# Kernel tuning notes

Measured on AMD Instinct MI355X. Metric: run time of the kernel, lower is better.

Reference implementation:

```python
import jax, jax.numpy as jnp
import numpy as np

O, T, DIN, H, DOUT = 50000, 500000, 128, 256, 128


def setup_inputs() -> dict:
    key = jax.random.key(0)
    ks = jax.random.split(key, 12)
    s = 0.05
    return {
        "obj_vecs": jax.random.normal(ks[0], (O, DIN), jnp.float32),
        "pred_vecs": jax.random.normal(ks[1], (T, DIN), jnp.float32),
        "edges": jax.random.randint(ks[2], (T, 2), 0, O, jnp.int64),
        "w1a": jax.random.normal(ks[3], (3 * DIN, H), jnp.float32) * s,
        "b1a": jax.random.normal(ks[4], (H,), jnp.float32) * s,
        "w1b": jax.random.normal(ks[5], (H, 2 * H + DOUT), jnp.float32) * s,
        "b1b": jax.random.normal(ks[6], (2 * H + DOUT,), jnp.float32) * s,
        "w2a": jax.random.normal(ks[7], (H, H), jnp.float32) * s,
        "b2a": jax.random.normal(ks[8], (H,), jnp.float32) * s,
        "w2b": jax.random.normal(ks[9], (H, DOUT), jnp.float32) * s,
        "b2b": jax.random.normal(ks[10], (DOUT,), jnp.float32) * s,
    }


def reference(obj_vecs, pred_vecs, edges, w1a, b1a, w1b, b1b, w2a, b2a, w2b, b2b):
    n_obj = obj_vecs.shape[0]
    h_dim = w2a.shape[0]
    d_out = w2b.shape[1]
    s_idx = edges[:, 0]
    o_idx = edges[:, 1]
    # gather subject/object node features, concat with predicate: [T, 3*Din]
    cur_t = jnp.concatenate([obj_vecs[s_idx], pred_vecs, obj_vecs[o_idx]], axis=1)
    # edge MLP (net1): Linear-ReLU-Linear-ReLU -> [T, 2H + Dout]
    new_t = jax.nn.relu(jax.nn.relu(cur_t @ w1a + b1a) @ w1b + b1b)
    new_s = new_t[:, :h_dim]
    new_p = new_t[:, h_dim:h_dim + d_out]
    new_o = new_t[:, h_dim + d_out:]
    # scatter-add pooling back to nodes, both endpoints
    idx = jnp.concatenate([s_idx, o_idx])
    vals = jnp.concatenate([new_s, new_o], axis=0)
    pooled = jax.ops.segment_sum(vals, idx, num_segments=n_obj)
    # avg pooling: divide by per-node incidence count (clamped to >= 1)
    counts = jax.ops.segment_sum(jnp.ones(idx.shape[0], obj_vecs.dtype), idx,
                                 num_segments=n_obj)
    pooled = pooled / jnp.clip(counts, 1.0)[:, None]
    # node MLP (net2)
    new_obj = jax.nn.relu(jax.nn.relu(pooled @ w2a + b2a) @ w2b + b2b)
    return new_obj, new_p
```

## Files before the change

### kernel.cpp

```cpp
#include <hip/hip_runtime.h>


using f32x4 = __attribute__((ext_vector_type(4))) float;
using s16x8 = __attribute__((ext_vector_type(8))) short;
typedef unsigned short u16x8 __attribute__((ext_vector_type(8)));

#define VMCNT4  asm volatile("s_waitcnt vmcnt(4)" ::: "memory")
#define VMCNT8  asm volatile("s_waitcnt vmcnt(8)" ::: "memory")
#define VMCNT16 asm volatile("s_waitcnt vmcnt(16)" ::: "memory")
#define VMCNT20 asm volatile("s_waitcnt vmcnt(20)" ::: "memory")
#define VMCNT36 asm volatile("s_waitcnt vmcnt(36)" ::: "memory")
#define LGKM0   asm volatile("s_waitcnt lgkmcnt(0)" ::: "memory")
#define BAR     __builtin_amdgcn_s_barrier()
#define SCHEDB  __builtin_amdgcn_sched_barrier(0)

static __device__ __forceinline__ unsigned short f2b(float f) {
    unsigned int u = __float_as_uint(f);
    unsigned int r = (u + 0x7fffu + ((u >> 16) & 1u)) >> 16;
    return (unsigned short)r;
}

static __device__ __forceinline__ unsigned f2bpk(float lo, float hi) {
    unsigned r;
    asm("v_cvt_pk_bf16_f32 %0, %1, %2" : "=v"(r) : "v"(lo), "v"(hi));
    return r;
}

static __device__ __forceinline__ float b2f(unsigned short b) {
    return __uint_as_float(((unsigned)b) << 16);
}

static __device__ __forceinline__ unsigned swz(unsigned row, unsigned byteoff) {
    return byteoff ^ ((row & 7u) << 4);
}

static __device__ __forceinline__ void gload_lds16(const unsigned short* g, unsigned short* l) {
    __builtin_amdgcn_global_load_lds(
        (const __attribute__((address_space(1))) unsigned int*)g,
        (__attribute__((address_space(3))) unsigned int*)l,
        16, 0, 0);
}

#define PREP_ELEMS (98304 + 163840 + 65536 + 32768)

__global__ void prep_count_kernel(const float* __restrict__ w1a, const float* __restrict__ w1b,
                                  const float* __restrict__ w2a, const float* __restrict__ w2b,
                                  unsigned short* __restrict__ w1aT, unsigned short* __restrict__ w1bT,
                                  unsigned short* __restrict__ w2aT, unsigned short* __restrict__ w2bT,
                                  const int* __restrict__ edges, int* __restrict__ cnt,
                                  int* __restrict__ slotS, int* __restrict__ slotO, int T) {
    int t = blockIdx.x * blockDim.x + threadIdx.x;
    if (t >= PREP_ELEMS) {
        int e = t - PREP_ELEMS;
        if (e < T) {
            slotS[e] = atomicAdd(&cnt[edges[2 * (long long)e]], 1);
            slotO[e] = atomicAdd(&cnt[edges[2 * (long long)e + 1]], 1);
        }
        return;
    }
    if (t < 6 * 16384) {
        int kt = t >> 14;
        int rem = t & 16383; int c = rem >> 6, kk = rem & 63;
        unsigned byte = ((unsigned)(c * 128 + kk * 2)) ^ ((c & 7u) << 4);
        *(unsigned short*)((char*)w1aT + (size_t)kt * 32768 + byte) =
            f2b(w1a[(size_t)(kt * 64 + kk) * 256 + c]);
        return;
    }
    t -= 98304;
    if (t < 10 * 16384) {
        int tile = t >> 14; int nc = tile >> 1, kh = tile & 1;
        int rem = t & 16383; int c = rem >> 7, kk = rem & 127;
        unsigned byte = ((unsigned)(c * 256 + kk * 2)) ^ ((c & 7u) << 4);
        *(unsigned short*)((char*)w1bT + (size_t)tile * 32768 + byte) =
            f2b(w1b[(size_t)(kh * 128 + kk) * 640 + nc * 128 + c]);
        return;
    }
    t -= 163840;
    if (t < 65536) { int n = t >> 8, k = t & 255; w2aT[t] = f2b(w2a[k * 256 + n]); return; }
    t -= 65536;
    if (t < 32768) { int n = t >> 8, k = t & 255; w2bT[t] = f2b(w2b[k * 128 + n]); return; }
}

__global__ void scan_kernel(const int* __restrict__ cnt, int* __restrict__ rowptr, int O) {
    __shared__ int sc[1024];
    const int tid = threadIdx.x;
    const int per = (O + 1023) >> 10;
    const int base = tid * per;
    int s = 0;
    for (int i = 0; i < per; ++i) { int j = base + i; if (j < O) s += cnt[j]; }
    sc[tid] = s;
    __syncthreads();
    for (int d = 1; d < 1024; d <<= 1) {
        int v = (tid >= d) ? sc[tid - d] : 0;
        __syncthreads();
        sc[tid] += v;
        __syncthreads();
    }
    int off = sc[tid] - s;
    for (int i = 0; i < per; ++i) {
        int j = base + i;
        if (j < O) { rowptr[j] = off; off += cnt[j]; }
    }
    if (tid == 0) rowptr[O] = sc[1023];
}

__global__ __launch_bounds__(512, 2) void edge_mlp(
    const float* __restrict__ obj, const float* __restrict__ pred,
    const int* __restrict__ edges,
    const unsigned short* __restrict__ w1aT, const float* __restrict__ b1a,
    const unsigned short* __restrict__ w1bT, const float* __restrict__ b1b,
    const int* __restrict__ slotS, const int* __restrict__ slotO,
    const int* __restrict__ rowptr,
    unsigned short* __restrict__ edgeout, float* __restrict__ outP, int T) {
    const int m0 = blockIdx.x * 128;
    const int tid = threadIdx.x;
    const int lane = tid & 63, wid = tid >> 6;
    const int wm = wid >> 2, wn = wid & 3;
    const bool evenL = ((lane & 1) == 0);

    __shared__ unsigned short U[81920];
    char* const ldsb = (char*)U;
    char* const bbase = ldsb + 65536;

    bool okR[4][4];
    #pragma unroll
    for (int mi = 0; mi < 4; ++mi)
        #pragma unroll
        for (int rr = 0; rr < 4; ++rr)
            okR[mi][rr] = (m0 + wm * 64 + mi * 16 + ((lane >> 4) << 2) + rr) < T;

    int slotSr[4][2], slotOr[4][2];
    #pragma unroll
    for (int mi = 0; mi < 4; ++mi)
        #pragma unroll
        for (int k = 0; k < 2; ++k) {
            int rsel = evenL ? k : 2 + k;
            int e = m0 + wm * 64 + mi * 16 + ((lane >> 4) << 2) + rsel;
            if (e >= T) e = T - 1;
            int si = edges[2 * (long long)e];
            int oi = edges[2 * (long long)e + 1];
            slotSr[mi][k] = slotS[e] + rowptr[si];
            slotOr[mi][k] = slotO[e] + rowptr[oi];
        }

    const int r = tid >> 2;
    const int q = tid & 3;
    int e_r = m0 + r; if (e_r >= T) e_r = T - 1;
    const int sIdx_r = edges[2 * (long long)e_r];
    const int oIdx_r = edges[2 * (long long)e_r + 1];

    float bias1[4], bias2[5][2];
    #pragma unroll
    for (int nj = 0; nj < 4; ++nj) bias1[nj] = b1a[wn * 64 + nj * 16 + (lane & 15)];
    #pragma unroll
    for (int nc = 0; nc < 5; ++nc)
        #pragma unroll
        for (int nj = 0; nj < 2; ++nj)
            bias2[nc][nj] = b1b[nc * 128 + wn * 32 + nj * 16 + (lane & 15)];

    #pragma unroll
    for (int mi = 0; mi < 4; ++mi)
        #pragma unroll
        for (int k = 0; k < 2; ++k)
            asm volatile("" :: "v"(slotSr[mi][k]), "v"(slotOr[mi][k]));
    #pragma unroll
    for (int nj = 0; nj < 4; ++nj) asm volatile("" :: "v"(bias1[nj]));
    #pragma unroll
    for (int nc = 0; nc < 5; ++nc)
        #pragma unroll
        for (int nj = 0; nj < 2; ++nj) asm volatile("" :: "v"(bias2[nc][nj]));
    asm volatile("" :: "v"((float)sIdx_r), "v"((float)oIdx_r));
    SCHEDB;

    auto aSrc = [&](int kt) -> const float4* {
        const float* s;
        if (kt < 2)      s = obj  + (long long)sIdx_r * 128 + kt * 64;
        else if (kt < 4) s = pred + (long long)e_r   * 128 + (kt - 2) * 64;
        else             s = obj  + (long long)oIdx_r * 128 + (kt - 4) * 64;
        return (const float4*)s;
    };

    auto tp = [&](int i) -> const unsigned short* {
        return (i < 6) ? (w1aT + (size_t)i * 16384) : (w1bT + (size_t)(i - 6) * 16384);
    };

    auto stage32 = [&](const unsigned short* gt, char* bb) {
        #pragma unroll
        for (int rr4 = 0; rr4 < 4; ++rr4) {
            unsigned off = wid * 4096u + rr4 * 1024u;
            gload_lds16((const unsigned short*)((const char*)gt + off + lane * 16u),
                        (unsigned short*)(bb + off));
        }
    };

    auto writeA = [&](const float4* ap, char* ab) {
        #pragma unroll
        for (int i = 0; i < 4; ++i) {
            float4 v = ap[i];
            uint2 pk;
            pk.x = f2bpk(v.x, v.y);
            pk.y = f2bpk(v.z, v.w);
            unsigned byte = (r * 128u + q * 32u + i * 8u) ^ ((r & 7u) << 4);
            *(uint2*)(ab + byte) = pk;
        }
    };

    f32x4 acc1[4][4];
    #pragma unroll
    for (int a = 0; a < 4; ++a)
        #pragma unroll
        for (int b = 0; b < 4; ++b) acc1[a][b] = f32x4{0.f, 0.f, 0.f, 0.f};

    auto mfma1 = [&](const char* ab, const char* bb) {
        #pragma unroll
        for (int ks = 0; ks < 2; ++ks) {
            const unsigned kk = ks * 32u + ((lane >> 4) << 3);
            s16x8 af[4];
            #pragma unroll
            for (int mi = 0; mi < 4; ++mi) {
                unsigned row = wm * 64u + mi * 16u + (lane & 15);
                af[mi] = *(const s16x8*)(ab + ((row * 128u + kk * 2u) ^ ((row & 7u) << 4)));
            }
            #pragma unroll
            for (int nj = 0; nj < 4; ++nj) {
                unsigned c = wn * 64u + nj * 16u + (lane & 15);
                s16x8 bf = *(const s16x8*)(bb + ((c * 128u + kk * 2u) ^ ((c & 7u) << 4)));
                #pragma unroll
                for (int mi = 0; mi < 4; ++mi)
                    acc1[mi][nj] = __builtin_amdgcn_mfma_f32_16x16x32_bf16(af[mi], bf, acc1[mi][nj], 0, 0, 0);
            }
        }
    };

    float4 ap[4];
    {
        const float4* s4 = aSrc(0);
        #pragma unroll
        for (int i = 0; i < 4; ++i) ap[i] = s4[q * 4 + i];
    }
    writeA(ap, ldsb);
    stage32(tp(0), bbase);
    stage32(tp(1), bbase + 32768);
    {
        const float4* s4 = aSrc(1);
        #pragma unroll
        for (int i = 0; i < 4; ++i) ap[i] = s4[q * 4 + i];
    }
    VMCNT8;
    LGKM0; BAR; SCHEDB;

    #pragma unroll
    for (int s = 0; s < 6; ++s) {
        stage32(tp(s + 2), bbase + ((s + 2) % 3) * 32768);
        __builtin_amdgcn_s_setprio(1);
        mfma1(ldsb + ((s >> 0) & 1) * 16384, bbase + (s % 3) * 32768);
        __builtin_amdgcn_s_setprio(0);
        VMCNT4;
        if (s < 5) {
            writeA(ap, ldsb + ((s + 1) & 1) * 16384);
            if (s < 4) {
                const float4* s4 = aSrc(s + 2);
                #pragma unroll
                for (int i = 0; i < 4; ++i) ap[i] = s4[q * 4 + i];
            }
        }
        LGKM0; BAR; SCHEDB;
    }

    #pragma unroll
    for (int nj = 0; nj < 4; ++nj) {
        unsigned col = wn * 64u + nj * 16u + (lane & 15);
        #pragma unroll
        for (int mi = 0; mi < 4; ++mi) {
            float r0 = fmaxf(acc1[mi][nj][0] + bias1[nj], 0.f);
            float r1 = fmaxf(acc1[mi][nj][1] + bias1[nj], 0.f);
            float r2 = fmaxf(acc1[mi][nj][2] + bias1[nj], 0.f);
            float r3 = fmaxf(acc1[mi][nj][3] + bias1[nj], 0.f);
            unsigned p01 = f2bpk(r0, r1);
            unsigned p23 = f2bpk(r2, r3);
            unsigned rowb = wm * 64u + mi * 16u + ((lane >> 4) << 2);
            *(unsigned short*)(ldsb + ((rowb * 512u + col * 2u) ^ ((rowb & 7u) << 4))) = (unsigned short)p01;
            *(unsigned short*)(ldsb + (((rowb + 1) * 512u + col * 2u) ^ (((rowb + 1) & 7u) << 4))) = (unsigned short)(p01 >> 16);
            *(unsigned short*)(ldsb + (((rowb + 2) * 512u + col * 2u) ^ (((rowb + 2) & 7u) << 4))) = (unsigned short)p23;
            *(unsigned short*)(ldsb + (((rowb + 3) * 512u + col * 2u) ^ (((rowb + 3) & 7u) << 4))) = (unsigned short)(p23 >> 16);
        }
    }
    LGKM0; BAR; SCHEDB;

    #pragma unroll
    for (int nc = 0; nc < 5; ++nc) {
        f32x4 acc2[4][2];
        #pragma unroll
        for (int a = 0; a < 4; ++a)
            #pragma unroll
            for (int b = 0; b < 2; ++b) acc2[a][b] = f32x4{0.f, 0.f, 0.f, 0.f};

        #pragma unroll
        for (int kh = 0; kh < 2; ++kh) {
            const int s = 6 + nc * 2 + kh;
            if (s + 2 <= 15) stage32(tp(s + 2), bbase + ((s + 2) % 3) * 32768);
            const char* bb = bbase + (s % 3) * 32768;
            __builtin_amdgcn_s_setprio(1);
            #pragma unroll
            for (int ks = 0; ks < 4; ++ks) {
                const unsigned kkB = ks * 32u + ((lane >> 4) << 3);
                const unsigned kkH = (kh * 128u) + kkB;
                s16x8 af[4];
                #pragma unroll
                for (int mi = 0; mi < 4; ++mi) {
                    unsigned row = wm * 64u + mi * 16u + (lane & 15);
                    af[mi] = *(const s16x8*)(ldsb + ((row * 512u + kkH * 2u) ^ ((row & 7u) << 4)));
                }
                #pragma unroll
                for (int nj = 0; nj < 2; ++nj) {
                    unsigned c = wn * 32u + nj * 16u + (lane & 15);
                    s16x8 bf = *(const s16x8*)(bb + ((c * 256u + kkB * 2u) ^ ((c & 7u) << 4)));
                    #pragma unroll
                    for (int mi = 0; mi < 4; ++mi)
                        acc2[mi][nj] = __builtin_amdgcn_mfma_f32_16x16x32_bf16(af[mi], bf, acc2[mi][nj], 0, 0, 0);
                }
            }
            __builtin_amdgcn_s_setprio(0);

            if (kh == 0) {
                if (s == 6)       { VMCNT4; }
                else if (s == 12) { VMCNT36; }
                else if (s == 14) { VMCNT16; }
                else              { VMCNT20; }
                LGKM0; BAR; SCHEDB;
            }
        }

        if (nc == 2) {
            #pragma unroll
            for (int nj = 0; nj < 2; ++nj) {
                int col = 2 * 128 + wn * 32 + nj * 16 + (lane & 15);
                #pragma unroll
                for (int mi = 0; mi < 4; ++mi)
                    #pragma unroll
                    for (int rr = 0; rr < 4; ++rr) {
                        int row = wm * 64 + mi * 16 + ((lane >> 4) << 2) + rr;
                        if (okR[mi][rr]) {
                            float v = acc2[mi][nj][rr] + bias2[2][nj];
                            v = v > 0.f ? v : 0.f;
                            outP[(long long)(m0 + row) * 128 + (col - 256)] = v;
                        }
                    }
            }
            VMCNT36;
            LGKM0; BAR; SCHEDB;
        } else {
            #pragma unroll
            for (int nj = 0; nj < 2; ++nj) {
                int col = nc * 128 + wn * 32 + nj * 16 + (lane & 15);
                int pc = (nc < 2) ? col : (col - 384);
                int pcb = (lane & 1) ? (pc - 1) : pc;
                #pragma unroll
                for (int mi = 0; mi < 4; ++mi) {
                    float vv[4];
                    #pragma unroll
                    for (int rr = 0; rr < 4; ++rr) {
                        float v = acc2[mi][nj][rr] + bias2[nc][nj];
                        vv[rr] = v > 0.f ? v : 0.f;
                    }
                    float nb0 = __shfl_xor(vv[0], 1);
                    float nb1 = __shfl_xor(vv[1], 1);
                    float nb2 = __shfl_xor(vv[2], 1);
                    float nb3 = __shfl_xor(vv[3], 1);
                    #pragma unroll
                    for (int k = 0; k < 2; ++k) {
                        float lo = evenL ? (k ? vv[1] : vv[0]) : (k ? nb3 : nb2);
                        float hi = evenL ? (k ? nb1 : nb0) : (k ? vv[3] : vv[2]);
                        int rsel = evenL ? k : 2 + k;
                        if (okR[mi][rsel]) {
                            int slot = (nc < 2) ? slotSr[mi][k] : slotOr[mi][k];
                            unsigned pk = f2bpk(lo, hi);
                            *(unsigned*)(edgeout + (size_t)slot * 256 + pcb) = pk;
                        }
                    }
                }
            }
            if (nc < 4) {
                VMCNT20;
                LGKM0; BAR; SCHEDB;
            }
        }
    }
}

__global__ __launch_bounds__(256, 3) void obj_mlp(
    const unsigned short* __restrict__ edgeout, const int* __restrict__ rowptr,
    const unsigned short* __restrict__ w2aT, const float* __restrict__ b2a,
    const unsigned short* __restrict__ w2bT, const float* __restrict__ b2b,
    float* __restrict__ outObj, int O) {
    const int m0 = blockIdx.x * 64;
    const int tid = threadIdx.x;
    const int lane = tid & 63, wid = tid >> 6;
    const int wm = wid >> 1, wn = wid & 1;

    __shared__ unsigned short Abuf[64 * 256];

    const int half = lane >> 5;
    const int coll = (lane & 31) * 8;
    for (int it = 0; it < 16; ++it) {
        const int row = it * 4 + wid;
        const int oI = m0 + row;
        float a0 = 0.f, a1 = 0.f, a2 = 0.f, a3 = 0.f, a4 = 0.f, a5 = 0.f, a6 = 0.f, a7 = 0.f;
        int n = 0;
        if (oI < O) {
            const int beg = rowptr[oI];
            n = rowptr[oI + 1] - beg;
            const unsigned short* base = edgeout + (size_t)beg * 256 + half * 256 + coll;
            int i = 0;
            for (; i + 7 < n; i += 8) {
                u16x8 v0 = *(const u16x8*)(base + (size_t)(i    ) * 256);
                u16x8 v1 = *(const u16x8*)(base + (size_t)(i + 2) * 256);
                u16x8 v2 = *(const u16x8*)(base + (size_t)(i + 4) * 256);
                u16x8 v3 = *(const u16x8*)(base + (size_t)(i + 6) * 256);
                a0 += b2f(v0[0]) + b2f(v1[0]) + b2f(v2[0]) + b2f(v3[0]);
                a1 += b2f(v0[1]) + b2f(v1[1]) + b2f(v2[1]) + b2f(v3[1]);
                a2 += b2f(v0[2]) + b2f(v1[2]) + b2f(v2[2]) + b2f(v3[2]);
                a3 += b2f(v0[3]) + b2f(v1[3]) + b2f(v2[3]) + b2f(v3[3]);
                a4 += b2f(v0[4]) + b2f(v1[4]) + b2f(v2[4]) + b2f(v3[4]);
                a5 += b2f(v0[5]) + b2f(v1[5]) + b2f(v2[5]) + b2f(v3[5]);
                a6 += b2f(v0[6]) + b2f(v1[6]) + b2f(v2[6]) + b2f(v3[6]);
                a7 += b2f(v0[7]) + b2f(v1[7]) + b2f(v2[7]) + b2f(v3[7]);
            }
            for (; i + 1 < n; i += 2) {
                u16x8 v0 = *(const u16x8*)(base + (size_t)i * 256);
                a0 += b2f(v0[0]); a1 += b2f(v0[1]); a2 += b2f(v0[2]); a3 += b2f(v0[3]);
                a4 += b2f(v0[4]); a5 += b2f(v0[5]); a6 += b2f(v0[6]); a7 += b2f(v0[7]);
            }
            if (i < n && half == 0) {
                u16x8 v0 = *(const u16x8*)(edgeout + (size_t)(beg + i) * 256 + coll);
                a0 += b2f(v0[0]); a1 += b2f(v0[1]); a2 += b2f(v0[2]); a3 += b2f(v0[3]);
                a4 += b2f(v0[4]); a5 += b2f(v0[5]); a6 += b2f(v0[6]); a7 += b2f(v0[7]);
            }
        }
        a0 += __shfl_xor(a0, 32); a1 += __shfl_xor(a1, 32);
        a2 += __shfl_xor(a2, 32); a3 += __shfl_xor(a3, 32);
        a4 += __shfl_xor(a4, 32); a5 += __shfl_xor(a5, 32);
        a6 += __shfl_xor(a6, 32); a7 += __shfl_xor(a7, 32);
        float inv = 1.f / fmaxf((float)n, 1.f);
        if (half == 0) {
            uint4 pk4;
            pk4.x = f2bpk(a0 * inv, a1 * inv);
            pk4.y = f2bpk(a2 * inv, a3 * inv);
            pk4.z = f2bpk(a4 * inv, a5 * inv);
            pk4.w = f2bpk(a6 * inv, a7 * inv);
            unsigned byte = ((unsigned)row * 512u + (unsigned)coll * 2u) ^ (((unsigned)row & 7u) << 4);
            *(uint4*)((char*)Abuf + byte) = pk4;
        }
    }
    __syncthreads();

    f32x4 acc1[2][2][4];
    #pragma unroll
    for (int a = 0; a < 2; ++a)
        #pragma unroll
        for (int b = 0; b < 2; ++b)
            #pragma unroll
            for (int c = 0; c < 4; ++c) acc1[a][b][c] = f32x4{0.f, 0.f, 0.f, 0.f};
    #pragma unroll
    for (int ks = 0; ks < 8; ++ks) {
        const int klane = ks * 32 + ((lane >> 4) << 3);
        s16x8 af[2];
        #pragma unroll
        for (int mi = 0; mi < 2; ++mi) {
            int row = wm * 32 + mi * 16 + (lane & 15);
            af[mi] = *(const s16x8*)((const char*)Abuf + swz(row, row * 512u + klane * 2u));
        }
        #pragma unroll
        for (int nb = 0; nb < 2; ++nb)
            #pragma unroll
            for (int nj = 0; nj < 4; ++nj) {
                int col = nb * 128 + wn * 64 + nj * 16 + (lane & 15);
                s16x8 bf = *(const s16x8*)(w2aT + (long long)col * 256 + klane);
                #pragma unroll
                for (int mi = 0; mi < 2; ++mi)
                    acc1[nb][mi][nj] = __builtin_amdgcn_mfma_f32_16x16x32_bf16(af[mi], bf, acc1[nb][mi][nj], 0, 0, 0);
            }
    }
    __syncthreads();

    #pragma unroll
    for (int nb = 0; nb < 2; ++nb)
        #pragma unroll
        for (int nj = 0; nj < 4; ++nj) {
            int col = nb * 128 + wn * 64 + nj * 16 + (lane & 15);
            float bias = b2a[col];
            #pragma unroll
            for (int mi = 0; mi < 2; ++mi) {
                float r0 = fmaxf(acc1[nb][mi][nj][0] + bias, 0.f);
                float r1 = fmaxf(acc1[nb][mi][nj][1] + bias, 0.f);
                float r2 = fmaxf(acc1[nb][mi][nj][2] + bias, 0.f);
                float r3 = fmaxf(acc1[nb][mi][nj][3] + bias, 0.f);
                unsigned p01 = f2bpk(r0, r1);
                unsigned p23 = f2bpk(r2, r3);
                int rowb = wm * 32 + mi * 16 + ((lane >> 4) << 2);
                *(unsigned short*)((char*)Abuf + swz(rowb, rowb * 512u + col * 2u)) = (unsigned short)p01;
                *(unsigned short*)((char*)Abuf + swz(rowb + 1, (rowb + 1) * 512u + col * 2u)) = (unsigned short)(p01 >> 16);
                *(unsigned short*)((char*)Abuf + swz(rowb + 2, (rowb + 2) * 512u + col * 2u)) = (unsigned short)p23;
                *(unsigned short*)((char*)Abuf + swz(rowb + 3, (rowb + 3) * 512u + col * 2u)) = (unsigned short)(p23 >> 16);
            }
        }
    __syncthreads();

    f32x4 acc2[2][4];
    #pragma unroll
    for (int b = 0; b < 2; ++b)
        #pragma unroll
        for (int c = 0; c < 4; ++c) acc2[b][c] = f32x4{0.f, 0.f, 0.f, 0.f};
    #pragma unroll
    for (int ks = 0; ks < 8; ++ks) {
        const int klane = ks * 32 + ((lane >> 4) << 3);
        s16x8 af[2];
        #pragma unroll
        for (int mi = 0; mi < 2; ++mi) {
            int row = wm * 32 + mi * 16 + (lane & 15);
            af[mi] = *(const s16x8*)((const char*)Abuf + swz(row, row * 512u + klane * 2u));
        }
        #pragma unroll
        for (int nj = 0; nj < 4; ++nj) {
            int col = wn * 64 + nj * 16 + (lane & 15);
            s16x8 bf = *(const s16x8*)(w2bT + (long long)col * 256 + klane);
            #pragma unroll
            for (int mi = 0; mi < 2; ++mi)
                acc2[mi][nj] = __builtin_amdgcn_mfma_f32_16x16x32_bf16(af[mi], bf, acc2[mi][nj], 0, 0, 0);
        }
    }

    #pragma unroll
    for (int nj = 0; nj < 4; ++nj) {
        int col = wn * 64 + nj * 16 + (lane & 15);
        float bias = b2b[col];
        #pragma unroll
        for (int mi = 0; mi < 2; ++mi)
            #pragma unroll
            for (int rr = 0; rr < 4; ++rr) {
                int row = wm * 32 + mi * 16 + ((lane >> 4) << 2) + rr;
                int o = m0 + row;
                if (o < O) {
                    float v = acc2[mi][nj][rr] + bias;
                    v = v > 0.f ? v : 0.f;
                    outObj[(long long)o * 128 + col] = v;
                }
            }
    }
}

extern "C" void kernel_launch(void* const* d_in, const int* in_sizes, int n_in,
                              void* d_out, int out_size, void* d_ws, size_t ws_size,
                              hipStream_t stream) {
    const float* obj  = (const float*)d_in[0];
    const float* pred = (const float*)d_in[1];
    const int*   edges = (const int*)d_in[2];
    const float* w1a = (const float*)d_in[3];
    const float* b1a = (const float*)d_in[4];
    const float* w1b = (const float*)d_in[5];
    const float* b1b = (const float*)d_in[6];
    const float* w2a = (const float*)d_in[7];
    const float* b2a = (const float*)d_in[8];
    const float* w2b = (const float*)d_in[9];
    const float* b2b = (const float*)d_in[10];

    const int O = in_sizes[0] / 128;
    const int T = in_sizes[1] / 128;

    auto al = [](size_t x) { return (x + 255) & ~(size_t)255; };
    const size_t szEdgeout = (size_t)2 * T * 256 * 2;
    const size_t szCnt     = (size_t)O * 4;
    const size_t szRow     = (size_t)(O + 1) * 4;
    const size_t szSlot    = (size_t)T * 4;

    size_t off = 0;
    char* ws = (char*)d_ws;
    unsigned short* edgeout = (unsigned short*)(ws + off); off += al(szEdgeout);
    int* cnt    = (int*)(ws + off); off += al(szCnt);
    int* rowptr = (int*)(ws + off); off += al(szRow);
    int* slotS  = (int*)(ws + off); off += al(szSlot);
    int* slotO  = (int*)(ws + off); off += al(szSlot);
    unsigned short* w1aT = (unsigned short*)(ws + off); off += (size_t)6 * 16384 * 2;
    unsigned short* w1bT = (unsigned short*)(ws + off); off += (size_t)10 * 16384 * 2;
    unsigned short* w2aT = (unsigned short*)(ws + off); off += (size_t)256 * 256 * 2;
    unsigned short* w2bT = (unsigned short*)(ws + off);

    float* outObj = (float*)d_out;
    float* outP   = (float*)d_out + (size_t)O * 128;

    hipMemsetAsync(cnt, 0, szCnt, stream);
    const int totalT = PREP_ELEMS + T;
    prep_count_kernel<<<(totalT + 255) / 256, 256, 0, stream>>>(
        w1a, w1b, w2a, w2b, w1aT, w1bT, w2aT, w2bT, edges, cnt, slotS, slotO, T);
    scan_kernel<<<1, 1024, 0, stream>>>(cnt, rowptr, O);
    edge_mlp<<<(T + 127) / 128, 512, 0, stream>>>(obj, pred, edges, w1aT, b1a, w1bT, b1b,
                                                  slotS, slotO, rowptr, edgeout, outP, T);
    obj_mlp<<<(O + 63) / 64, 256, 0, stream>>>(edgeout, rowptr, w2aT, b2a, w2bT, b2b, outObj, O);
}
```

Before: 868.1 us.

## Split pooling gather out of obj_mlp into a separate high-occupancy kernel

Moves the segment-average gather over edge outputs out of obj_mlp into a new pool_gather kernel. That kernel runs one wave per object at launch bounds allowing 8 blocks per CU and writes pooled bf16 rows to a workspace buffer. obj_mlp then only loads the pooled rows into swizzled LDS before its GEMMs. The aim is to hide the latency of the irregular gather with more parallelism than the 3-block-per-CU MLP kernel can offer. The cost is an extra launch plus writing and re-reading an O×256 bf16 intermediate.

```diff
diff --git a/kernel.cpp b/kernel.cpp
--- a/kernel.cpp
+++ b/kernel.cpp
@@ -253,7 +253,7 @@
     for (int s = 0; s < 6; ++s) {
         stage32(tp(s + 2), bbase + ((s + 2) % 3) * 32768);
         __builtin_amdgcn_s_setprio(1);
-        mfma1(ldsb + ((s >> 0) & 1) * 16384, bbase + (s % 3) * 32768);
+        mfma1(ldsb + (s & 1) * 16384, bbase + (s % 3) * 32768);
         __builtin_amdgcn_s_setprio(0);
         VMCNT4;
         if (s < 5) {
@@ -388,8 +388,61 @@
     }
 }
 
+__global__ __launch_bounds__(256, 8) void pool_gather(
+    const unsigned short* __restrict__ edgeout, const int* __restrict__ rowptr,
+    unsigned short* __restrict__ pooled, int O) {
+    const int w = blockIdx.x * 4 + (threadIdx.x >> 6);
+    if (w >= O) return;
+    const int lane = threadIdx.x & 63;
+    const int half = lane >> 5;
+    const int coll = (lane & 31) * 8;
+
+    const int beg = rowptr[w];
+    const int n = rowptr[w + 1] - beg;
+    float a0 = 0.f, a1 = 0.f, a2 = 0.f, a3 = 0.f, a4 = 0.f, a5 = 0.f, a6 = 0.f, a7 = 0.f;
+    const unsigned short* base = edgeout + (size_t)beg * 256 + half * 256 + coll;
+    int i = 0;
+    for (; i + 7 < n; i += 8) {
+        u16x8 v0 = *(const u16x8*)(base + (size_t)(i    ) * 256);
+        u16x8 v1 = *(const u16x8*)(base + (size_t)(i + 2) * 256);
+        u16x8 v2 = *(const u16x8*)(base + (size_t)(i + 4) * 256);
+        u16x8 v3 = *(const u16x8*)(base + (size_t)(i + 6) * 256);
+        a0 += b2f(v0[0]) + b2f(v1[0]) + b2f(v2[0]) + b2f(v3[0]);
+        a1 += b2f(v0[1]) + b2f(v1[1]) + b2f(v2[1]) + b2f(v3[1]);
+        a2 += b2f(v0[2]) + b2f(v1[2]) + b2f(v2[2]) + b2f(v3[2]);
+        a3 += b2f(v0[3]) + b2f(v1[3]) + b2f(v2[3]) + b2f(v3[3]);
+        a4 += b2f(v0[4]) + b2f(v1[4]) + b2f(v2[4]) + b2f(v3[4]);
+        a5 += b2f(v0[5]) + b2f(v1[5]) + b2f(v2[5]) + b2f(v3[5]);
+        a6 += b2f(v0[6]) + b2f(v1[6]) + b2f(v2[6]) + b2f(v3[6]);
+        a7 += b2f(v0[7]) + b2f(v1[7]) + b2f(v2[7]) + b2f(v3[7]);
+    }
+    for (; i + 1 < n; i += 2) {
+        u16x8 v0 = *(const u16x8*)(base + (size_t)i * 256);
+        a0 += b2f(v0[0]); a1 += b2f(v0[1]); a2 += b2f(v0[2]); a3 += b2f(v0[3]);
+        a4 += b2f(v0[4]); a5 += b2f(v0[5]); a6 += b2f(v0[6]); a7 += b2f(v0[7]);
+    }
+    if (i < n && half == 0) {
+        u16x8 v0 = *(const u16x8*)(edgeout + (size_t)(beg + i) * 256 + coll);
+        a0 += b2f(v0[0]); a1 += b2f(v0[1]); a2 += b2f(v0[2]); a3 += b2f(v0[3]);
+        a4 += b2f(v0[4]); a5 += b2f(v0[5]); a6 += b2f(v0[6]); a7 += b2f(v0[7]);
+    }
+    a0 += __shfl_xor(a0, 32); a1 += __shfl_xor(a1, 32);
+    a2 += __shfl_xor(a2, 32); a3 += __shfl_xor(a3, 32);
+    a4 += __shfl_xor(a4, 32); a5 += __shfl_xor(a5, 32);
+    a6 += __shfl_xor(a6, 32); a7 += __shfl_xor(a7, 32);
+    float inv = 1.f / fmaxf((float)n, 1.f);
+    if (half == 0) {
+        uint4 pk4;
+        pk4.x = f2bpk(a0 * inv, a1 * inv);
+        pk4.y = f2bpk(a2 * inv, a3 * inv);
+        pk4.z = f2bpk(a4 * inv, a5 * inv);
+        pk4.w = f2bpk(a6 * inv, a7 * inv);
+        *(uint4*)(pooled + (size_t)w * 256 + coll) = pk4;
+    }
+}
+
 __global__ __launch_bounds__(256, 3) void obj_mlp(
-    const unsigned short* __restrict__ edgeout, const int* __restrict__ rowptr,
+    const unsigned short* __restrict__ pooled,
     const unsigned short* __restrict__ w2aT, const float* __restrict__ b2a,
     const unsigned short* __restrict__ w2bT, const float* __restrict__ b2b,
     float* __restrict__ outObj, int O) {
@@ -400,56 +453,15 @@
 
     __shared__ unsigned short Abuf[64 * 256];
 
-    const int half = lane >> 5;
-    const int coll = (lane & 31) * 8;
-    for (int it = 0; it < 16; ++it) {
-        const int row = it * 4 + wid;
-        const int oI = m0 + row;
-        float a0 = 0.f, a1 = 0.f, a2 = 0.f, a3 = 0.f, a4 = 0.f, a5 = 0.f, a6 = 0.f, a7 = 0.f;
-        int n = 0;
-        if (oI < O) {
-            const int beg = rowptr[oI];
-            n = rowptr[oI + 1] - beg;
-            const unsigned short* base = edgeout + (size_t)beg * 256 + half * 256 + coll;
-            int i = 0;
-            for (; i + 7 < n; i += 8) {
-                u16x8 v0 = *(const u16x8*)(base + (size_t)(i    ) * 256);
-                u16x8 v1 = *(const u16x8*)(base + (size_t)(i + 2) * 256);
-                u16x8 v2 = *(const u16x8*)(base + (size_t)(i + 4) * 256);
-                u16x8 v3 = *(const u16x8*)(base + (size_t)(i + 6) * 256);
-                a0 += b2f(v0[0]) + b2f(v1[0]) + b2f(v2[0]) + b2f(v3[0]);
-                a1 += b2f(v0[1]) + b2f(v1[1]) + b2f(v2[1]) + b2f(v3[1]);
-                a2 += b2f(v0[2]) + b2f(v1[2]) + b2f(v2[2]) + b2f(v3[2]);
-                a3 += b2f(v0[3]) + b2f(v1[3]) + b2f(v2[3]) + b2f(v3[3]);
-                a4 += b2f(v0[4]) + b2f(v1[4]) + b2f(v2[4]) + b2f(v3[4]);
-                a5 += b2f(v0[5]) + b2f(v1[5]) + b2f(v2[5]) + b2f(v3[5]);
-                a6 += b2f(v0[6]) + b2f(v1[6]) + b2f(v2[6]) + b2f(v3[6]);
-                a7 += b2f(v0[7]) + b2f(v1[7]) + b2f(v2[7]) + b2f(v3[7]);
-            }
-            for (; i + 1 < n; i += 2) {
-                u16x8 v0 = *(const u16x8*)(base + (size_t)i * 256);
-                a0 += b2f(v0[0]); a1 += b2f(v0[1]); a2 += b2f(v0[2]); a3 += b2f(v0[3]);
-                a4 += b2f(v0[4]); a5 += b2f(v0[5]); a6 += b2f(v0[6]); a7 += b2f(v0[7]);
-            }
-            if (i < n && half == 0) {
-                u16x8 v0 = *(const u16x8*)(edgeout + (size_t)(beg + i) * 256 + coll);
-                a0 += b2f(v0[0]); a1 += b2f(v0[1]); a2 += b2f(v0[2]); a3 += b2f(v0[3]);
-                a4 += b2f(v0[4]); a5 += b2f(v0[5]); a6 += b2f(v0[6]); a7 += b2f(v0[7]);
-            }
-        }
-        a0 += __shfl_xor(a0, 32); a1 += __shfl_xor(a1, 32);
-        a2 += __shfl_xor(a2, 32); a3 += __shfl_xor(a3, 32);
-        a4 += __shfl_xor(a4, 32); a5 += __shfl_xor(a5, 32);
-        a6 += __shfl_xor(a6, 32); a7 += __shfl_xor(a7, 32);
-        float inv = 1.f / fmaxf((float)n, 1.f);
-        if (half == 0) {
-            uint4 pk4;
-            pk4.x = f2bpk(a0 * inv, a1 * inv);
-            pk4.y = f2bpk(a2 * inv, a3 * inv);
-            pk4.z = f2bpk(a4 * inv, a5 * inv);
-            pk4.w = f2bpk(a6 * inv, a7 * inv);
-            unsigned byte = ((unsigned)row * 512u + (unsigned)coll * 2u) ^ (((unsigned)row & 7u) << 4);
-            *(uint4*)((char*)Abuf + byte) = pk4;
+    {
+        const int r = tid >> 2, q = tid & 3;
+        int objc = m0 + r; if (objc >= O) objc = O - 1;
+        const u16x8* s8 = (const u16x8*)(pooled + (size_t)objc * 256);
+        #pragma unroll
+        for (int i = 0; i < 8; ++i) {
+            u16x8 v = s8[q * 8 + i];
+            unsigned byte = r * 512u + (q * 64u + i * 8u) * 2u;
+            *(u16x8*)((char*)Abuf + swz(r, byte)) = v;
         }
     }
     __syncthreads();
@@ -569,6 +581,7 @@
 
     auto al = [](size_t x) { return (x + 255) & ~(size_t)255; };
     const size_t szEdgeout = (size_t)2 * T * 256 * 2;
+    const size_t szPooled  = (size_t)O * 256 * 2;
     const size_t szCnt     = (size_t)O * 4;
     const size_t szRow     = (size_t)(O + 1) * 4;
     const size_t szSlot    = (size_t)T * 4;
@@ -576,6 +589,7 @@
     size_t off = 0;
     char* ws = (char*)d_ws;
     unsigned short* edgeout = (unsigned short*)(ws + off); off += al(szEdgeout);
+    unsigned short* pooled  = (unsigned short*)(ws + off); off += al(szPooled);
     int* cnt    = (int*)(ws + off); off += al(szCnt);
     int* rowptr = (int*)(ws + off); off += al(szRow);
     int* slotS  = (int*)(ws + off); off += al(szSlot);
@@ -595,5 +609,6 @@
     scan_kernel<<<1, 1024, 0, stream>>>(cnt, rowptr, O);
     edge_mlp<<<(T + 127) / 128, 512, 0, stream>>>(obj, pred, edges, w1aT, b1a, w1bT, b1b,
                                                   slotS, slotO, rowptr, edgeout, outP, T);
-    obj_mlp<<<(O + 63) / 64, 256, 0, stream>>>(edgeout, rowptr, w2aT, b2a, w2bT, b2b, outObj, O);
-}
+    pool_gather<<<(O + 3) / 4, 256, 0, stream>>>(edgeout, rowptr, pooled, O);
+    obj_mlp<<<(O + 63) / 64, 256, 0, stream>>>(pooled, w2aT, b2a, w2bT, b2b, outObj, O);
+}
```

After: 832.6 us. 4.1% less time.
